# Optimization experiments

Measured on AMD Instinct MI355X. Metric: run time of the kernel, lower is better.

Reference implementation:

```python
import jax, jax.numpy as jnp
import numpy as np

N = 50000   # nodes
E = 600000  # edges
D = 128     # in_feats
H = 128     # n_hidden
C = 47      # n_classes


def setup_inputs() -> dict:
    key = jax.random.key(0)
    ks = jax.random.split(key, 12)
    x = jax.random.normal(ks[0], (N, D), dtype=jnp.float32)
    src = jax.random.randint(ks[1], (E,), 0, N, dtype=jnp.int32)
    dst = jax.random.randint(ks[2], (E,), 0, N, dtype=jnp.int32)
    def lin(k, fi, fo):
        s = 1.0 / np.sqrt(fi)
        return jax.random.uniform(k, (fi, fo), jnp.float32, -s, s)
    return {
        "x": x, "src": src, "dst": dst,
        "W_self0": lin(ks[3], D, H), "W_neigh0": lin(ks[4], D, H), "b0": jnp.zeros((H,), jnp.float32),
        "W_self1": lin(ks[5], H, H), "W_neigh1": lin(ks[6], H, H), "b1": jnp.zeros((H,), jnp.float32),
        "W_self2": lin(ks[7], H, C), "W_neigh2": lin(ks[8], H, C), "b2": jnp.zeros((C,), jnp.float32),
    }


def _sage_layer(h, src, dst, W_self, W_neigh, b, act):
    # gather neighbor (src) features, mean-aggregate onto dst nodes
    msum = jax.ops.segment_sum(h[src], dst, num_segments=N)           # [N, F]
    deg = jax.ops.segment_sum(jnp.ones((src.shape[0], 1), h.dtype), dst, num_segments=N)
    h_neigh = msum / jnp.maximum(deg, 1.0)                            # zero-degree -> 0
    out = h @ W_self + h_neigh @ W_neigh + b
    return jax.nn.relu(out) if act else out


def reference(x, src, dst, W_self0, W_neigh0, b0, W_self1, W_neigh1, b1, W_self2, W_neigh2, b2):
    h = _sage_layer(x, src, dst, W_self0, W_neigh0, b0, True)
    h = _sage_layer(h, src, dst, W_self1, W_neigh1, b1, True)
    h = _sage_layer(h, src, dst, W_self2, W_neigh2, b2, False)
    return h
```

## Files before the change

kernel.cpp:

```cpp
#include <hip/hip_runtime.h>
#include <hip/hip_bf16.h>


#define THREADS 256

typedef unsigned short u16;
typedef __attribute__((ext_vector_type(8))) short bf16x8;
typedef __attribute__((ext_vector_type(4))) float f32x4;

__device__ inline u16 f2bf(float f) {
    union { float f; unsigned u; } v; v.f = f;
    unsigned r = (v.u + 0x7FFFu + ((v.u >> 16) & 1u)) >> 16;
    return (u16)r;
}
__device__ inline float bf2f(u16 b) {
    union { unsigned u; float f; } v; v.u = ((unsigned)b) << 16;
    return v.f;
}
__device__ inline unsigned pack2(float a, float b) {
    return (unsigned)f2bf(a) | ((unsigned)f2bf(b) << 16);
}

#define GLDS16(gp, lp)                                                         \
    __builtin_amdgcn_global_load_lds(                                          \
        (const __attribute__((address_space(1))) void*)(gp),                   \
        (__attribute__((address_space(3))) void*)(lp), 16, 0, 0)

__global__ void k_count(const int* __restrict__ dst, int* __restrict__ deg, int E) {
    int e = blockIdx.x * blockDim.x + threadIdx.x;
    if (e < E) atomicAdd(&deg[dst[e]], 1);
}

__global__ void k_scan_block(const int* __restrict__ deg, int* __restrict__ off,
                             int* __restrict__ bsum, int n) {
    __shared__ int s[256];
    int t = threadIdx.x;
    int base = blockIdx.x * 1024 + t * 4;
    int v[4];
#pragma unroll
    for (int i = 0; i < 4; i++) v[i] = (base + i < n) ? deg[base + i] : 0;
    int sum = v[0] + v[1] + v[2] + v[3];
    int val = sum;
    s[t] = val;
    __syncthreads();
    for (int o = 1; o < 256; o <<= 1) {
        int x = (t >= o) ? s[t - o] : 0;
        __syncthreads();
        val += x;
        s[t] = val;
        __syncthreads();
    }
    int run = val - sum;
#pragma unroll
    for (int i = 0; i < 4; i++) {
        if (base + i < n) off[base + i] = run;
        run += v[i];
    }
    if (t == 255) bsum[blockIdx.x] = val;
}

__global__ void k_scan_bsum(int* __restrict__ bsum, int nb) {
    int lane = threadIdx.x;
    int carry = 0;
    for (int start = 0; start < nb; start += 64) {
        int i = start + lane;
        int orig = (i < nb) ? bsum[i] : 0;
        int v = orig;
#pragma unroll
        for (int o = 1; o < 64; o <<= 1) {
            int u = __shfl_up(v, o, 64);
            if (lane >= o) v += u;
        }
        if (i < nb) bsum[i] = carry + v - orig;
        carry += __shfl(v, 63, 64);
    }
}

__global__ void k_scan_add(int* __restrict__ off, const int* __restrict__ bsum, int n) {
    int t = threadIdx.x;
    int base = blockIdx.x * 1024 + t * 4;
    int add = bsum[blockIdx.x];
#pragma unroll
    for (int i = 0; i < 4; i++)
        if (base + i < n) off[base + i] += add;
}

__global__ void k_fill(const int* __restrict__ src, const int* __restrict__ dst,
                       const int* __restrict__ off, int* __restrict__ cur,
                       int* __restrict__ eidx, int E) {
    int e = blockIdx.x * blockDim.x + threadIdx.x;
    if (e < E) {
        int d = dst[e];
        int p = atomicAdd(&cur[d], 1);
        eidx[off[d] + p] = src[e];
    }
}

__global__ void k_prepX(const float* __restrict__ x, u16* __restrict__ hi,
                        u16* __restrict__ lo, int n32) {
    int i = blockIdx.x * blockDim.x + threadIdx.x;
    if (i >= n32) return;
    float4 v = ((const float4*)x)[i];
    float h0 = bf2f(f2bf(v.x)), h1 = bf2f(f2bf(v.y)), h2 = bf2f(f2bf(v.z)), h3 = bf2f(f2bf(v.w));
    uint2 hp, lp;
    hp.x = pack2(h0, h1); hp.y = pack2(h2, h3);
    lp.x = pack2(v.x - h0, v.y - h1); lp.y = pack2(v.z - h2, v.w - h3);
    ((uint2*)hi)[i] = hp;
    ((uint2*)lo)[i] = lp;
}

__global__ void k_prepW3(const float* __restrict__ Ws0, const float* __restrict__ Wn0,
                         const float* __restrict__ Ws1, const float* __restrict__ Wn1,
                         const float* __restrict__ Ws2, const float* __restrict__ Wn2,
                         u16* __restrict__ Bt) {
    int idx = blockIdx.x * blockDim.x + threadIdx.x;
    if (idx >= 3 * 128 * 256) return;
    int layer = idx >> 15;
    int within = idx & 32767;
    int col = within >> 8;
    int k = within & 255;
    const float* Ws = (layer == 0) ? Ws0 : (layer == 1) ? Ws1 : Ws2;
    const float* Wn = (layer == 0) ? Wn0 : (layer == 1) ? Wn1 : Wn2;
    int fout = (layer == 2) ? 47 : 128;
    float v = 0.f;
    if (col < fout) v = (k < 128) ? Ws[k * fout + col] : Wn[(k - 128) * fout + col];
    u16 h = f2bf(v);
    Bt[layer * 65536 + within] = h;
    Bt[layer * 65536 + 32768 + within] = f2bf(v - bf2f(h));
}

__global__ void k_aggregate(const u16* __restrict__ hi_in, const int* __restrict__ eidx,
                            const int* __restrict__ off, const int* __restrict__ deg,
                            u16* __restrict__ mhi, u16* __restrict__ mlo, int n) {
    int wv = blockIdx.x * 4 + (threadIdx.x >> 6);
    int lane = threadIdx.x & 63;
    int half = lane >> 5;
    int hl = lane & 31;
    int node = wv * 2 + half;
    if (node >= n) return;
    int cnt = deg[node];
    int base = off[node];
    const uint2* h2 = (const uint2*)hi_in;
    float4 acc = make_float4(0.f, 0.f, 0.f, 0.f);
    for (int j = 0; j < cnt; j += 8) {
        int s[8];
        float m[8];
#pragma unroll
        for (int u = 0; u < 8; u++) {
            int jj = j + u;
            s[u] = eidx[base + (jj < cnt ? jj : 0)];
            m[u] = (jj < cnt) ? 1.f : 0.f;
        }
        uint2 v[8];
#pragma unroll
        for (int u = 0; u < 8; u++) v[u] = h2[(size_t)s[u] * 32 + hl];
#pragma unroll
        for (int u = 0; u < 8; u++) {
            acc.x = fmaf(m[u], bf2f((u16)(v[u].x & 0xffffu)), acc.x);
            acc.y = fmaf(m[u], bf2f((u16)(v[u].x >> 16)), acc.y);
            acc.z = fmaf(m[u], bf2f((u16)(v[u].y & 0xffffu)), acc.z);
            acc.w = fmaf(m[u], bf2f((u16)(v[u].y >> 16)), acc.w);
        }
    }
    float iv = 1.0f / (float)(cnt > 1 ? cnt : 1);
    float a0 = acc.x * iv, a1 = acc.y * iv, a2 = acc.z * iv, a3 = acc.w * iv;
    float r0 = bf2f(f2bf(a0)), r1 = bf2f(f2bf(a1)), r2 = bf2f(f2bf(a2)), r3 = bf2f(f2bf(a3));
    uint2 hp, lp;
    hp.x = pack2(a0, a1); hp.y = pack2(a2, a3);
    lp.x = pack2(a0 - r0, a1 - r1); lp.y = pack2(a2 - r2, a3 - r3);
    ((uint2*)mhi)[(size_t)node * 32 + hl] = hp;
    ((uint2*)mlo)[(size_t)node * 32 + hl] = lp;
}

__global__ __launch_bounds__(256) void k_gemm_mfma(
    const u16* __restrict__ Ahi_s, const u16* __restrict__ Alo_s,
    const u16* __restrict__ Ahi_n, const u16* __restrict__ Alo_n,
    const u16* __restrict__ Bthi, const u16* __restrict__ Btlo,
    const float* __restrict__ bias, float* __restrict__ out_f32,
    u16* __restrict__ out_hi, u16* __restrict__ out_lo, int n, int fout, int relu) {
    __shared__ u16 sAhi[64 * 32];
    __shared__ u16 sAlo[64 * 32];
    __shared__ u16 sBhi[128 * 32];
    __shared__ u16 sBlo[128 * 32];

    int t = threadIdx.x;
    int w = t >> 6;
    int lane = t & 63;
    int wr = w >> 1, wc = w & 1;
    size_t row0 = (size_t)blockIdx.x * 64;

    f32x4 acc[2][4];
#pragma unroll
    for (int r = 0; r < 2; r++)
#pragma unroll
        for (int c = 0; c < 4; c++) acc[r][c] = (f32x4){0.f, 0.f, 0.f, 0.f};

    for (int kk = 0; kk < 256; kk += 32) {
        const u16* Phi = (kk < 128) ? Ahi_s : Ahi_n;
        const u16* Plo = (kk < 128) ? Alo_s : Alo_n;
        int kc = kk & 127;
        __syncthreads();
        {
            int r = w * 16 + (lane >> 2);
            int cb = (lane & 3) * 8;
            GLDS16(Phi + (row0 + r) * 128 + kc + cb, &sAhi[r * 32 + cb]);
            GLDS16(Plo + (row0 + r) * 128 + kc + cb, &sAlo[r * 32 + cb]);
        }
#pragma unroll
        for (int i = 0; i < 2; i++) {
            int c = w * 32 + i * 16 + (lane >> 2);
            int cb = (lane & 3) * 8;
            GLDS16(Bthi + (size_t)c * 256 + kk + cb, &sBhi[c * 32 + cb]);
            GLDS16(Btlo + (size_t)c * 256 + kk + cb, &sBlo[c * 32 + cb]);
        }
        __syncthreads();

        bf16x8 a_hi[2], a_lo[2], b_hi[4], b_lo[4];
        int q8 = (lane >> 4) * 8;
#pragma unroll
        for (int r = 0; r < 2; r++) {
            int ad = (wr * 32 + r * 16 + (lane & 15)) * 32 + q8;
            a_hi[r] = *(const bf16x8*)&sAhi[ad];
            a_lo[r] = *(const bf16x8*)&sAlo[ad];
        }
#pragma unroll
        for (int c = 0; c < 4; c++) {
            int ad = (wc * 64 + c * 16 + (lane & 15)) * 32 + q8;
            b_hi[c] = *(const bf16x8*)&sBhi[ad];
            b_lo[c] = *(const bf16x8*)&sBlo[ad];
        }
#pragma unroll
        for (int r = 0; r < 2; r++)
#pragma unroll
            for (int c = 0; c < 4; c++) {
                acc[r][c] = __builtin_amdgcn_mfma_f32_16x16x32_bf16(
                    a_hi[r], b_hi[c], acc[r][c], 0, 0, 0);
                acc[r][c] = __builtin_amdgcn_mfma_f32_16x16x32_bf16(
                    a_hi[r], b_lo[c], acc[r][c], 0, 0, 0);
                acc[r][c] = __builtin_amdgcn_mfma_f32_16x16x32_bf16(
                    a_lo[r], b_hi[c], acc[r][c], 0, 0, 0);
            }
    }

    int quad = lane >> 4;
    int lcol = lane & 15;
#pragma unroll
    for (int r = 0; r < 2; r++) {
#pragma unroll
        for (int c = 0; c < 4; c++) {
            int col = wc * 64 + c * 16 + lcol;
            float bv = (col < fout) ? bias[col] : 0.f;
#pragma unroll
            for (int g = 0; g < 4; g++) {
                size_t row = row0 + wr * 32 + r * 16 + quad * 4 + g;
                if (row >= (size_t)n || col >= fout) continue;
                float v = acc[r][c][g] + bv;
                if (relu) v = v > 0.f ? v : 0.f;
                if (out_f32) out_f32[row * fout + col] = v;
                if (out_hi) {
                    u16 h = f2bf(v);
                    out_hi[row * 128 + col] = h;
                    out_lo[row * 128 + col] = f2bf(v - bf2f(h));
                }
            }
        }
    }
}

extern "C" void kernel_launch(void* const* d_in, const int* in_sizes, int n_in,
                              void* d_out, int out_size, void* d_ws, size_t ws_size,
                              hipStream_t stream) {
    const float* x = (const float*)d_in[0];
    const int* src = (const int*)d_in[1];
    const int* dst = (const int*)d_in[2];
    const float* Ws0 = (const float*)d_in[3];
    const float* Wn0 = (const float*)d_in[4];
    const float* b0 = (const float*)d_in[5];
    const float* Ws1 = (const float*)d_in[6];
    const float* Wn1 = (const float*)d_in[7];
    const float* b1 = (const float*)d_in[8];
    const float* Ws2 = (const float*)d_in[9];
    const float* Wn2 = (const float*)d_in[10];
    const float* b2 = (const float*)d_in[11];
    float* out = (float*)d_out;

    const int N = in_sizes[0] / 128;
    const int E = in_sizes[1];
    const int Npad = ((N + 63) / 64) * 64;

    char* p = (char*)d_ws;
    u16* P0hi = (u16*)p; p += (size_t)Npad * 128 * 2;
    u16* P0lo = (u16*)p; p += (size_t)Npad * 128 * 2;
    u16* P1hi = (u16*)p; p += (size_t)Npad * 128 * 2;
    u16* P1lo = (u16*)p; p += (size_t)Npad * 128 * 2;
    u16* Mhi = (u16*)p; p += (size_t)Npad * 128 * 2;
    u16* Mlo = (u16*)p; p += (size_t)Npad * 128 * 2;
    u16* Bt = (u16*)p; p += 3 * 2 * 128 * 256 * 2;
    int* deg = (int*)p; p += (size_t)N * 4;
    int* cur = (int*)p; p += (size_t)N * 4;
    int* off = (int*)p; p += (size_t)N * 4;
    int* eidx = (int*)p; p += (size_t)E * 4;
    int* bsum = (int*)p;

    const int nbE = (E + THREADS - 1) / THREADS;
    const int nbScan = (N + 1023) / 1024;
    const int nbAgg = (N + 7) / 8;
    const int nbGemm = (N + 63) / 64;
    const int nbPX = (N * 32 + THREADS - 1) / THREADS;
    const int nbPW = (3 * 128 * 256 + THREADS - 1) / THREADS;

    hipMemsetAsync(deg, 0, (size_t)2 * N * sizeof(int), stream);

    k_count<<<nbE, THREADS, 0, stream>>>(dst, deg, E);
    k_scan_block<<<nbScan, 256, 0, stream>>>(deg, off, bsum, N);
    k_scan_bsum<<<1, 64, 0, stream>>>(bsum, nbScan);
    k_scan_add<<<nbScan, 256, 0, stream>>>(off, bsum, N);
    k_fill<<<nbE, THREADS, 0, stream>>>(src, dst, off, cur, eidx, E);

    k_prepX<<<nbPX, THREADS, 0, stream>>>(x, P0hi, P0lo, N * 32);
    k_prepW3<<<nbPW, THREADS, 0, stream>>>(Ws0, Wn0, Ws1, Wn1, Ws2, Wn2, Bt);

    k_aggregate<<<nbAgg, 256, 0, stream>>>(P0hi, eidx, off, deg, Mhi, Mlo, N);
    k_gemm_mfma<<<nbGemm, 256, 0, stream>>>(P0hi, P0lo, Mhi, Mlo,
                                            Bt + 0 * 65536, Bt + 0 * 65536 + 32768, b0,
                                            (float*)nullptr, P1hi, P1lo, N, 128, 1);
    k_aggregate<<<nbAgg, 256, 0, stream>>>(P1hi, eidx, off, deg, Mhi, Mlo, N);
    k_gemm_mfma<<<nbGemm, 256, 0, stream>>>(P1hi, P1lo, Mhi, Mlo,
                                            Bt + 1 * 65536, Bt + 1 * 65536 + 32768, b1,
                                            (float*)nullptr, P0hi, P0lo, N, 128, 1);
    k_aggregate<<<nbAgg, 256, 0, stream>>>(P0hi, eidx, off, deg, Mhi, Mlo, N);
    k_gemm_mfma<<<nbGemm, 256, 0, stream>>>(P0hi, P0lo, Mhi, Mlo,
                                            Bt + 2 * 65536, Bt + 2 * 65536 + 32768, b2,
                                            out, (u16*)nullptr, (u16*)nullptr, N, 47, 0);
}
```

Measured before the change: 309.2 us.

## Fuse all stages into one cooperative persistent kernel with grid syncs

Replaces the sequence of separate kernel launches (memset, degree count, scans, CSR fill, prep, and per-layer aggregate/GEMM) with a single cooperative kernel that runs each stage in grid-stride loops separated by grid-wide barriers. The goal is to remove the launch overhead and inter-kernel gaps of roughly a dozen small launches. The cost is that the grid is capped at 1024 blocks, so the aggregation and GEMM stages lose occupancy compared with the previous oversubscribed grids. The grid barriers add their own cost, and the block-sum scan now uses a serial prefix loop per chunk.

```diff
diff --git a/kernel.cpp b/kernel.cpp
--- a/kernel.cpp
+++ b/kernel.cpp
@@ -1,8 +1,9 @@
 #include <hip/hip_runtime.h>
 #include <hip/hip_bf16.h>
-
-
-#define THREADS 256
+#include <hip/hip_cooperative_groups.h>
+
+namespace cg = cooperative_groups;
+
 
 typedef unsigned short u16;
 typedef __attribute__((ext_vector_type(8))) short bf16x8;
@@ -26,264 +27,266 @@
         (const __attribute__((address_space(1))) void*)(gp),                   \
         (__attribute__((address_space(3))) void*)(lp), 16, 0, 0)
 
-__global__ void k_count(const int* __restrict__ dst, int* __restrict__ deg, int E) {
-    int e = blockIdx.x * blockDim.x + threadIdx.x;
-    if (e < E) atomicAdd(&deg[dst[e]], 1);
-}
-
-__global__ void k_scan_block(const int* __restrict__ deg, int* __restrict__ off,
-                             int* __restrict__ bsum, int n) {
-    __shared__ int s[256];
-    int t = threadIdx.x;
-    int base = blockIdx.x * 1024 + t * 4;
-    int v[4];
-#pragma unroll
-    for (int i = 0; i < 4; i++) v[i] = (base + i < n) ? deg[base + i] : 0;
-    int sum = v[0] + v[1] + v[2] + v[3];
-    int val = sum;
-    s[t] = val;
-    __syncthreads();
-    for (int o = 1; o < 256; o <<= 1) {
-        int x = (t >= o) ? s[t - o] : 0;
+struct MegaParams {
+    const float* x;
+    const int* src;
+    const int* dst;
+    const float *Ws0, *Wn0, *b0, *Ws1, *Wn1, *b1, *Ws2, *Wn2, *b2;
+    float* out;
+    u16 *P0hi, *P0lo, *P1hi, *P1lo, *Mhi, *Mlo, *Bt;
+    int *deg, *cur, *off, *eidx, *bsum;
+    int N, E, nscan, ntiles;
+};
+
+union SmemU {
+    struct {
+        u16 Ahi[64 * 32];
+        u16 Alo[64 * 32];
+        u16 Bhi[128 * 32];
+        u16 Blo[128 * 32];
+    } g;
+    int scan[256];
+};
+
+__global__ __launch_bounds__(256, 4) void k_mega(MegaParams P) {
+    cg::grid_group grid = cg::this_grid();
+    __shared__ __align__(16) SmemU S;
+
+    const int t = threadIdx.x;
+    const int G = gridDim.x;
+    const int gtid = blockIdx.x * 256 + t;
+    const int nthr = G * 256;
+    const int w = t >> 6;
+    const int lane = t & 63;
+    const int wr = w >> 1, wc = w & 1;
+
+    for (int i = gtid; i < 2 * P.N; i += nthr) P.deg[i] = 0;
+    grid.sync();
+
+    for (int e = gtid; e < P.E; e += nthr) atomicAdd(&P.deg[P.dst[e]], 1);
+    for (int i = gtid; i < P.N * 32; i += nthr) {
+        float4 v = ((const float4*)P.x)[i];
+        float h0 = bf2f(f2bf(v.x)), h1 = bf2f(f2bf(v.y));
+        float h2 = bf2f(f2bf(v.z)), h3 = bf2f(f2bf(v.w));
+        uint2 hp, lp;
+        hp.x = pack2(h0, h1); hp.y = pack2(h2, h3);
+        lp.x = pack2(v.x - h0, v.y - h1); lp.y = pack2(v.z - h2, v.w - h3);
+        ((uint2*)P.P0hi)[i] = hp;
+        ((uint2*)P.P0lo)[i] = lp;
+    }
+    for (int idx = gtid; idx < 3 * 128 * 256; idx += nthr) {
+        int layer = idx >> 15;
+        int within = idx & 32767;
+        int col = within >> 8;
+        int k = within & 255;
+        const float* Ws = (layer == 0) ? P.Ws0 : (layer == 1) ? P.Ws1 : P.Ws2;
+        const float* Wn = (layer == 0) ? P.Wn0 : (layer == 1) ? P.Wn1 : P.Wn2;
+        int fo = (layer == 2) ? 47 : 128;
+        float v = 0.f;
+        if (col < fo) v = (k < 128) ? Ws[k * fo + col] : Wn[(k - 128) * fo + col];
+        u16 h = f2bf(v);
+        P.Bt[layer * 65536 + within] = h;
+        P.Bt[layer * 65536 + 32768 + within] = f2bf(v - bf2f(h));
+    }
+    grid.sync();
+
+    for (int chunk = blockIdx.x; chunk < P.nscan; chunk += G) {
+        int base = chunk * 1024 + t * 4;
+        int v[4];
+#pragma unroll
+        for (int i = 0; i < 4; i++) v[i] = (base + i < P.N) ? P.deg[base + i] : 0;
+        int sum = v[0] + v[1] + v[2] + v[3];
+        int val = sum;
+        S.scan[t] = val;
         __syncthreads();
-        val += x;
-        s[t] = val;
+        for (int o = 1; o < 256; o <<= 1) {
+            int x = (t >= o) ? S.scan[t - o] : 0;
+            __syncthreads();
+            val += x;
+            S.scan[t] = val;
+            __syncthreads();
+        }
+        int run = val - sum;
+#pragma unroll
+        for (int i = 0; i < 4; i++) {
+            if (base + i < P.N) P.off[base + i] = run;
+            run += v[i];
+        }
+        if (t == 255) P.bsum[chunk] = val;
         __syncthreads();
     }
-    int run = val - sum;
-#pragma unroll
-    for (int i = 0; i < 4; i++) {
-        if (base + i < n) off[base + i] = run;
-        run += v[i];
-    }
-    if (t == 255) bsum[blockIdx.x] = val;
-}
-
-__global__ void k_scan_bsum(int* __restrict__ bsum, int nb) {
-    int lane = threadIdx.x;
-    int carry = 0;
-    for (int start = 0; start < nb; start += 64) {
-        int i = start + lane;
-        int orig = (i < nb) ? bsum[i] : 0;
-        int v = orig;
-#pragma unroll
-        for (int o = 1; o < 64; o <<= 1) {
-            int u = __shfl_up(v, o, 64);
-            if (lane >= o) v += u;
+    grid.sync();
+
+    for (int chunk = blockIdx.x; chunk < P.nscan; chunk += G) {
+        int add = 0;
+        for (int j = 0; j < chunk; j++) add += P.bsum[j];
+        int base = chunk * 1024 + t * 4;
+#pragma unroll
+        for (int i = 0; i < 4; i++)
+            if (base + i < P.N) P.off[base + i] += add;
+    }
+    grid.sync();
+
+    for (int e = gtid; e < P.E; e += nthr) {
+        int d = P.dst[e];
+        int p = atomicAdd(&P.cur[d], 1);
+        P.eidx[P.off[d] + p] = P.src[e];
+    }
+    grid.sync();
+
+    const u16* aggIn[3] = {P.P0hi, P.P1hi, P.P0hi};
+    const u16* Ahis[3] = {P.P0hi, P.P1hi, P.P0hi};
+    const u16* Alos[3] = {P.P0lo, P.P1lo, P.P0lo};
+    u16* Ohi[3] = {P.P1hi, P.P0hi, nullptr};
+    u16* Olo[3] = {P.P1lo, P.P0lo, nullptr};
+    const float* biasL[3] = {P.b0, P.b1, P.b2};
+
+    for (int layer = 0; layer < 3; layer++) {
+        {
+            const uint2* h2 = (const uint2*)aggIn[layer];
+            int half = lane >> 5;
+            int hl = lane & 31;
+            int gw = blockIdx.x * 4 + w;
+            int gwaves = G * 4;
+            int ntask = (P.N + 1) >> 1;
+            for (int task = gw; task < ntask; task += gwaves) {
+                int node = task * 2 + half;
+                if (node >= P.N) continue;
+                int cnt = P.deg[node];
+                int base = P.off[node];
+                float4 acc = make_float4(0.f, 0.f, 0.f, 0.f);
+                for (int j = 0; j < cnt; j += 8) {
+                    int s[8];
+                    float m[8];
+#pragma unroll
+                    for (int u = 0; u < 8; u++) {
+                        int jj = j + u;
+                        s[u] = P.eidx[base + (jj < cnt ? jj : 0)];
+                        m[u] = (jj < cnt) ? 1.f : 0.f;
+                    }
+                    uint2 v[8];
+#pragma unroll
+                    for (int u = 0; u < 8; u++) v[u] = h2[(size_t)s[u] * 32 + hl];
+#pragma unroll
+                    for (int u = 0; u < 8; u++) {
+                        acc.x = fmaf(m[u], bf2f((u16)(v[u].x & 0xffffu)), acc.x);
+                        acc.y = fmaf(m[u], bf2f((u16)(v[u].x >> 16)), acc.y);
+                        acc.z = fmaf(m[u], bf2f((u16)(v[u].y & 0xffffu)), acc.z);
+                        acc.w = fmaf(m[u], bf2f((u16)(v[u].y >> 16)), acc.w);
+                    }
+                }
+                float iv = 1.0f / (float)(cnt > 1 ? cnt : 1);
+                float a0 = acc.x * iv, a1 = acc.y * iv, a2 = acc.z * iv, a3 = acc.w * iv;
+                float r0 = bf2f(f2bf(a0)), r1 = bf2f(f2bf(a1));
+                float r2 = bf2f(f2bf(a2)), r3 = bf2f(f2bf(a3));
+                uint2 hp, lp;
+                hp.x = pack2(a0, a1); hp.y = pack2(a2, a3);
+                lp.x = pack2(a0 - r0, a1 - r1); lp.y = pack2(a2 - r2, a3 - r3);
+                ((uint2*)P.Mhi)[(size_t)node * 32 + hl] = hp;
+                ((uint2*)P.Mlo)[(size_t)node * 32 + hl] = lp;
+            }
         }
-        if (i < nb) bsum[i] = carry + v - orig;
-        carry += __shfl(v, 63, 64);
-    }
-}
-
-__global__ void k_scan_add(int* __restrict__ off, const int* __restrict__ bsum, int n) {
-    int t = threadIdx.x;
-    int base = blockIdx.x * 1024 + t * 4;
-    int add = bsum[blockIdx.x];
-#pragma unroll
-    for (int i = 0; i < 4; i++)
-        if (base + i < n) off[base + i] += add;
-}
-
-__global__ void k_fill(const int* __restrict__ src, const int* __restrict__ dst,
-                       const int* __restrict__ off, int* __restrict__ cur,
-                       int* __restrict__ eidx, int E) {
-    int e = blockIdx.x * blockDim.x + threadIdx.x;
-    if (e < E) {
-        int d = dst[e];
-        int p = atomicAdd(&cur[d], 1);
-        eidx[off[d] + p] = src[e];
-    }
-}
-
-__global__ void k_prepX(const float* __restrict__ x, u16* __restrict__ hi,
-                        u16* __restrict__ lo, int n32) {
-    int i = blockIdx.x * blockDim.x + threadIdx.x;
-    if (i >= n32) return;
-    float4 v = ((const float4*)x)[i];
-    float h0 = bf2f(f2bf(v.x)), h1 = bf2f(f2bf(v.y)), h2 = bf2f(f2bf(v.z)), h3 = bf2f(f2bf(v.w));
-    uint2 hp, lp;
-    hp.x = pack2(h0, h1); hp.y = pack2(h2, h3);
-    lp.x = pack2(v.x - h0, v.y - h1); lp.y = pack2(v.z - h2, v.w - h3);
-    ((uint2*)hi)[i] = hp;
-    ((uint2*)lo)[i] = lp;
-}
-
-__global__ void k_prepW3(const float* __restrict__ Ws0, const float* __restrict__ Wn0,
-                         const float* __restrict__ Ws1, const float* __restrict__ Wn1,
-                         const float* __restrict__ Ws2, const float* __restrict__ Wn2,
-                         u16* __restrict__ Bt) {
-    int idx = blockIdx.x * blockDim.x + threadIdx.x;
-    if (idx >= 3 * 128 * 256) return;
-    int layer = idx >> 15;
-    int within = idx & 32767;
-    int col = within >> 8;
-    int k = within & 255;
-    const float* Ws = (layer == 0) ? Ws0 : (layer == 1) ? Ws1 : Ws2;
-    const float* Wn = (layer == 0) ? Wn0 : (layer == 1) ? Wn1 : Wn2;
-    int fout = (layer == 2) ? 47 : 128;
-    float v = 0.f;
-    if (col < fout) v = (k < 128) ? Ws[k * fout + col] : Wn[(k - 128) * fout + col];
-    u16 h = f2bf(v);
-    Bt[layer * 65536 + within] = h;
-    Bt[layer * 65536 + 32768 + within] = f2bf(v - bf2f(h));
-}
-
-__global__ void k_aggregate(const u16* __restrict__ hi_in, const int* __restrict__ eidx,
-                            const int* __restrict__ off, const int* __restrict__ deg,
-                            u16* __restrict__ mhi, u16* __restrict__ mlo, int n) {
-    int wv = blockIdx.x * 4 + (threadIdx.x >> 6);
-    int lane = threadIdx.x & 63;
-    int half = lane >> 5;
-    int hl = lane & 31;
-    int node = wv * 2 + half;
-    if (node >= n) return;
-    int cnt = deg[node];
-    int base = off[node];
-    const uint2* h2 = (const uint2*)hi_in;
-    float4 acc = make_float4(0.f, 0.f, 0.f, 0.f);
-    for (int j = 0; j < cnt; j += 8) {
-        int s[8];
-        float m[8];
-#pragma unroll
-        for (int u = 0; u < 8; u++) {
-            int jj = j + u;
-            s[u] = eidx[base + (jj < cnt ? jj : 0)];
-            m[u] = (jj < cnt) ? 1.f : 0.f;
-        }
-        uint2 v[8];
-#pragma unroll
-        for (int u = 0; u < 8; u++) v[u] = h2[(size_t)s[u] * 32 + hl];
-#pragma unroll
-        for (int u = 0; u < 8; u++) {
-            acc.x = fmaf(m[u], bf2f((u16)(v[u].x & 0xffffu)), acc.x);
-            acc.y = fmaf(m[u], bf2f((u16)(v[u].x >> 16)), acc.y);
-            acc.z = fmaf(m[u], bf2f((u16)(v[u].y & 0xffffu)), acc.z);
-            acc.w = fmaf(m[u], bf2f((u16)(v[u].y >> 16)), acc.w);
-        }
-    }
-    float iv = 1.0f / (float)(cnt > 1 ? cnt : 1);
-    float a0 = acc.x * iv, a1 = acc.y * iv, a2 = acc.z * iv, a3 = acc.w * iv;
-    float r0 = bf2f(f2bf(a0)), r1 = bf2f(f2bf(a1)), r2 = bf2f(f2bf(a2)), r3 = bf2f(f2bf(a3));
-    uint2 hp, lp;
-    hp.x = pack2(a0, a1); hp.y = pack2(a2, a3);
-    lp.x = pack2(a0 - r0, a1 - r1); lp.y = pack2(a2 - r2, a3 - r3);
-    ((uint2*)mhi)[(size_t)node * 32 + hl] = hp;
-    ((uint2*)mlo)[(size_t)node * 32 + hl] = lp;
-}
-
-__global__ __launch_bounds__(256) void k_gemm_mfma(
-    const u16* __restrict__ Ahi_s, const u16* __restrict__ Alo_s,
-    const u16* __restrict__ Ahi_n, const u16* __restrict__ Alo_n,
-    const u16* __restrict__ Bthi, const u16* __restrict__ Btlo,
-    const float* __restrict__ bias, float* __restrict__ out_f32,
-    u16* __restrict__ out_hi, u16* __restrict__ out_lo, int n, int fout, int relu) {
-    __shared__ u16 sAhi[64 * 32];
-    __shared__ u16 sAlo[64 * 32];
-    __shared__ u16 sBhi[128 * 32];
-    __shared__ u16 sBlo[128 * 32];
-
-    int t = threadIdx.x;
-    int w = t >> 6;
-    int lane = t & 63;
-    int wr = w >> 1, wc = w & 1;
-    size_t row0 = (size_t)blockIdx.x * 64;
-
-    f32x4 acc[2][4];
-#pragma unroll
-    for (int r = 0; r < 2; r++)
-#pragma unroll
-        for (int c = 0; c < 4; c++) acc[r][c] = (f32x4){0.f, 0.f, 0.f, 0.f};
-
-    for (int kk = 0; kk < 256; kk += 32) {
-        const u16* Phi = (kk < 128) ? Ahi_s : Ahi_n;
-        const u16* Plo = (kk < 128) ? Alo_s : Alo_n;
-        int kc = kk & 127;
-        __syncthreads();
+        grid.sync();
+
         {
-            int r = w * 16 + (lane >> 2);
-            int cb = (lane & 3) * 8;
-            GLDS16(Phi + (row0 + r) * 128 + kc + cb, &sAhi[r * 32 + cb]);
-            GLDS16(Plo + (row0 + r) * 128 + kc + cb, &sAlo[r * 32 + cb]);
-        }
-#pragma unroll
-        for (int i = 0; i < 2; i++) {
-            int c = w * 32 + i * 16 + (lane >> 2);
-            int cb = (lane & 3) * 8;
-            GLDS16(Bthi + (size_t)c * 256 + kk + cb, &sBhi[c * 32 + cb]);
-            GLDS16(Btlo + (size_t)c * 256 + kk + cb, &sBlo[c * 32 + cb]);
-        }
-        __syncthreads();
-
-        bf16x8 a_hi[2], a_lo[2], b_hi[4], b_lo[4];
-        int q8 = (lane >> 4) * 8;
-#pragma unroll
-        for (int r = 0; r < 2; r++) {
-            int ad = (wr * 32 + r * 16 + (lane & 15)) * 32 + q8;
-            a_hi[r] = *(const bf16x8*)&sAhi[ad];
-            a_lo[r] = *(const bf16x8*)&sAlo[ad];
-        }
-#pragma unroll
-        for (int c = 0; c < 4; c++) {
-            int ad = (wc * 64 + c * 16 + (lane & 15)) * 32 + q8;
-            b_hi[c] = *(const bf16x8*)&sBhi[ad];
-            b_lo[c] = *(const bf16x8*)&sBlo[ad];
-        }
-#pragma unroll
-        for (int r = 0; r < 2; r++)
-#pragma unroll
-            for (int c = 0; c < 4; c++) {
-                acc[r][c] = __builtin_amdgcn_mfma_f32_16x16x32_bf16(
-                    a_hi[r], b_hi[c], acc[r][c], 0, 0, 0);
-                acc[r][c] = __builtin_amdgcn_mfma_f32_16x16x32_bf16(
-                    a_hi[r], b_lo[c], acc[r][c], 0, 0, 0);
-                acc[r][c] = __builtin_amdgcn_mfma_f32_16x16x32_bf16(
-                    a_lo[r], b_hi[c], acc[r][c], 0, 0, 0);
-            }
-    }
-
-    int quad = lane >> 4;
-    int lcol = lane & 15;
-#pragma unroll
-    for (int r = 0; r < 2; r++) {
-#pragma unroll
-        for (int c = 0; c < 4; c++) {
-            int col = wc * 64 + c * 16 + lcol;
-            float bv = (col < fout) ? bias[col] : 0.f;
-#pragma unroll
-            for (int g = 0; g < 4; g++) {
-                size_t row = row0 + wr * 32 + r * 16 + quad * 4 + g;
-                if (row >= (size_t)n || col >= fout) continue;
-                float v = acc[r][c][g] + bv;
-                if (relu) v = v > 0.f ? v : 0.f;
-                if (out_f32) out_f32[row * fout + col] = v;
-                if (out_hi) {
-                    u16 h = f2bf(v);
-                    out_hi[row * 128 + col] = h;
-                    out_lo[row * 128 + col] = f2bf(v - bf2f(h));
+            const u16* Ahi_s = Ahis[layer];
+            const u16* Alo_s = Alos[layer];
+            const u16* Bthi = P.Bt + layer * 65536;
+            const u16* Btlo = Bthi + 32768;
+            const float* bias = biasL[layer];
+            u16* out_hi = Ohi[layer];
+            u16* out_lo = Olo[layer];
+            float* out_f32 = (layer == 2) ? P.out : nullptr;
+            int fout = (layer == 2) ? 47 : 128;
+            int relu = (layer < 2) ? 1 : 0;
+
+            for (int tile = blockIdx.x; tile < P.ntiles; tile += G) {
+                size_t row0 = (size_t)tile * 64;
+                f32x4 acc[2][4];
+#pragma unroll
+                for (int r = 0; r < 2; r++)
+#pragma unroll
+                    for (int c = 0; c < 4; c++) acc[r][c] = (f32x4){0.f, 0.f, 0.f, 0.f};
+
+                for (int kk = 0; kk < 256; kk += 32) {
+                    const u16* Phi = (kk < 128) ? Ahi_s : P.Mhi;
+                    const u16* Plo = (kk < 128) ? Alo_s : P.Mlo;
+                    int kc = kk & 127;
+                    __syncthreads();
+                    {
+                        int r = w * 16 + (lane >> 2);
+                        int cb = (lane & 3) * 8;
+                        GLDS16(Phi + (row0 + r) * 128 + kc + cb, &S.g.Ahi[r * 32 + cb]);
+                        GLDS16(Plo + (row0 + r) * 128 + kc + cb, &S.g.Alo[r * 32 + cb]);
+                    }
+#pragma unroll
+                    for (int i = 0; i < 2; i++) {
+                        int c = w * 32 + i * 16 + (lane >> 2);
+                        int cb = (lane & 3) * 8;
+                        GLDS16(Bthi + (size_t)c * 256 + kk + cb, &S.g.Bhi[c * 32 + cb]);
+                        GLDS16(Btlo + (size_t)c * 256 + kk + cb, &S.g.Blo[c * 32 + cb]);
+                    }
+                    __syncthreads();
+
+                    bf16x8 a_hi[2], a_lo[2], b_hi[4], b_lo[4];
+                    int q8 = (lane >> 4) * 8;
+#pragma unroll
+                    for (int r = 0; r < 2; r++) {
+                        int ad = (wr * 32 + r * 16 + (lane & 15)) * 32 + q8;
+                        a_hi[r] = *(const bf16x8*)&S.g.Ahi[ad];
+                        a_lo[r] = *(const bf16x8*)&S.g.Alo[ad];
+                    }
+#pragma unroll
+                    for (int c = 0; c < 4; c++) {
+                        int ad = (wc * 64 + c * 16 + (lane & 15)) * 32 + q8;
+                        b_hi[c] = *(const bf16x8*)&S.g.Bhi[ad];
+                        b_lo[c] = *(const bf16x8*)&S.g.Blo[ad];
+                    }
+#pragma unroll
+                    for (int r = 0; r < 2; r++)
+#pragma unroll
+                        for (int c = 0; c < 4; c++) {
+                            acc[r][c] = __builtin_amdgcn_mfma_f32_16x16x32_bf16(
+                                a_hi[r], b_hi[c], acc[r][c], 0, 0, 0);
+                            acc[r][c] = __builtin_amdgcn_mfma_f32_16x16x32_bf16(
+                                a_hi[r], b_lo[c], acc[r][c], 0, 0, 0);
+                            acc[r][c] = __builtin_amdgcn_mfma_f32_16x16x32_bf16(
+                                a_lo[r], b_hi[c], acc[r][c], 0, 0, 0);
+                        }
+                }
+
+                int quad = lane >> 4;
+                int lcol = lane & 15;
+#pragma unroll
+                for (int r = 0; r < 2; r++) {
+#pragma unroll
+                    for (int c = 0; c < 4; c++) {
+                        int col = wc * 64 + c * 16 + lcol;
+                        float bv = (col < fout) ? bias[col] : 0.f;
+#pragma unroll
+                        for (int g = 0; g < 4; g++) {
+                            size_t row = row0 + wr * 32 + r * 16 + quad * 4 + g;
+                            if (row >= (size_t)P.N || col >= fout) continue;
+                            float v = acc[r][c][g] + bv;
+                            if (relu) v = v > 0.f ? v : 0.f;
+                            if (out_f32) out_f32[row * fout + col] = v;
+                            if (out_hi) {
+                                u16 h = f2bf(v);
+                                out_hi[row * 128 + col] = h;
+                                out_lo[row * 128 + col] = f2bf(v - bf2f(h));
+                            }
+                        }
+                    }
                 }
             }
         }
+        if (layer < 2) grid.sync();
     }
 }
 
 extern "C" void kernel_launch(void* const* d_in, const int* in_sizes, int n_in,
                               void* d_out, int out_size, void* d_ws, size_t ws_size,
                               hipStream_t stream) {
-    const float* x = (const float*)d_in[0];
-    const int* src = (const int*)d_in[1];
-    const int* dst = (const int*)d_in[2];
-    const float* Ws0 = (const float*)d_in[3];
-    const float* Wn0 = (const float*)d_in[4];
-    const float* b0 = (const float*)d_in[5];
-    const float* Ws1 = (const float*)d_in[6];
-    const float* Wn1 = (const float*)d_in[7];
-    const float* b1 = (const float*)d_in[8];
-    const float* Ws2 = (const float*)d_in[9];
-    const float* Wn2 = (const float*)d_in[10];
-    const float* b2 = (const float*)d_in[11];
-    float* out = (float*)d_out;
-
     const int N = in_sizes[0] / 128;
     const int E = in_sizes[1];
     const int Npad = ((N + 63) / 64) * 64;
@@ -302,34 +305,40 @@
     int* eidx = (int*)p; p += (size_t)E * 4;
     int* bsum = (int*)p;
 
-    const int nbE = (E + THREADS - 1) / THREADS;
-    const int nbScan = (N + 1023) / 1024;
-    const int nbAgg = (N + 7) / 8;
-    const int nbGemm = (N + 63) / 64;
-    const int nbPX = (N * 32 + THREADS - 1) / THREADS;
-    const int nbPW = (3 * 128 * 256 + THREADS - 1) / THREADS;
-
-    hipMemsetAsync(deg, 0, (size_t)2 * N * sizeof(int), stream);
-
-    k_count<<<nbE, THREADS, 0, stream>>>(dst, deg, E);
-    k_scan_block<<<nbScan, 256, 0, stream>>>(deg, off, bsum, N);
-    k_scan_bsum<<<1, 64, 0, stream>>>(bsum, nbScan);
-    k_scan_add<<<nbScan, 256, 0, stream>>>(off, bsum, N);
-    k_fill<<<nbE, THREADS, 0, stream>>>(src, dst, off, cur, eidx, E);
-
-    k_prepX<<<nbPX, THREADS, 0, stream>>>(x, P0hi, P0lo, N * 32);
-    k_prepW3<<<nbPW, THREADS, 0, stream>>>(Ws0, Wn0, Ws1, Wn1, Ws2, Wn2, Bt);
-
-    k_aggregate<<<nbAgg, 256, 0, stream>>>(P0hi, eidx, off, deg, Mhi, Mlo, N);
-    k_gemm_mfma<<<nbGemm, 256, 0, stream>>>(P0hi, P0lo, Mhi, Mlo,
-                                            Bt + 0 * 65536, Bt + 0 * 65536 + 32768, b0,
-                                            (float*)nullptr, P1hi, P1lo, N, 128, 1);
-    k_aggregate<<<nbAgg, 256, 0, stream>>>(P1hi, eidx, off, deg, Mhi, Mlo, N);
-    k_gemm_mfma<<<nbGemm, 256, 0, stream>>>(P1hi, P1lo, Mhi, Mlo,
-                                            Bt + 1 * 65536, Bt + 1 * 65536 + 32768, b1,
-                                            (float*)nullptr, P0hi, P0lo, N, 128, 1);
-    k_aggregate<<<nbAgg, 256, 0, stream>>>(P0hi, eidx, off, deg, Mhi, Mlo, N);
-    k_gemm_mfma<<<nbGemm, 256, 0, stream>>>(P0hi, P0lo, Mhi, Mlo,
-                                            Bt + 2 * 65536, Bt + 2 * 65536 + 32768, b2,
-                                            out, (u16*)nullptr, (u16*)nullptr, N, 47, 0);
-}
+    MegaParams mp;
+    mp.x = (const float*)d_in[0];
+    mp.src = (const int*)d_in[1];
+    mp.dst = (const int*)d_in[2];
+    mp.Ws0 = (const float*)d_in[3];
+    mp.Wn0 = (const float*)d_in[4];
+    mp.b0 = (const float*)d_in[5];
+    mp.Ws1 = (const float*)d_in[6];
+    mp.Wn1 = (const float*)d_in[7];
+    mp.b1 = (const float*)d_in[8];
+    mp.Ws2 = (const float*)d_in[9];
+    mp.Wn2 = (const float*)d_in[10];
+    mp.b2 = (const float*)d_in[11];
+    mp.out = (float*)d_out;
+    mp.P0hi = P0hi; mp.P0lo = P0lo;
+    mp.P1hi = P1hi; mp.P1lo = P1lo;
+    mp.Mhi = Mhi; mp.Mlo = Mlo;
+    mp.Bt = Bt;
+    mp.deg = deg; mp.cur = cur; mp.off = off; mp.eidx = eidx; mp.bsum = bsum;
+    mp.N = N;
+    mp.E = E;
+    mp.nscan = (N + 1023) / 1024;
+    mp.ntiles = (N + 63) / 64;
+
+    int blocksPerCU = 0;
+    hipOccupancyMaxActiveBlocksPerMultiprocessor(&blocksPerCU, (const void*)k_mega,
+                                                 256, 0);
+    if (blocksPerCU < 1) blocksPerCU = 1;
+    int numCU = 256;
+    hipDeviceGetAttribute(&numCU, hipDeviceAttributeMultiprocessorCount, 0);
+    int G = blocksPerCU * numCU;
+    if (G > 1024) G = 1024;
+
+    void* kargs[] = {(void*)&mp};
+    hipLaunchCooperativeKernel((const void*)k_mega, dim3(G), dim3(256), kargs,
+                               0, stream);
+}
```

Result: slower. 1.055 ms (+241.1%).
